# Optimization experiments

Measured on AMD Instinct MI355X. Metric: run time of the kernel, lower is better.

Reference implementation:

```python
import jax, jax.numpy as jnp
import numpy as np

N, DIM, DK, DV = 8192, 1024, 128, 128


def setup_inputs() -> dict:
    key = jax.random.key(0)
    ks = jax.random.split(key, 5)
    # Match equinox Linear init scale roughly (uniform(-1/sqrt(in), 1/sqrt(in)))
    lim = 1.0 / np.sqrt(DIM)
    return {
        "x": jax.random.normal(ks[0], (N, DIM), dtype=jnp.float32),
        "Wqk": jax.random.uniform(ks[1], (DK, DIM), jnp.float32, -lim, lim),
        "bqk": jax.random.uniform(ks[2], (DK,), jnp.float32, -lim, lim),
        "Wv": jax.random.uniform(ks[3], (DV, DIM), jnp.float32, -lim, lim),
        "bv": jax.random.uniform(ks[4], (DV,), jnp.float32, -lim, lim),
    }


def reference(x, Wqk, bqk, Wv, bv):
    # shared QK projection: q == k == x @ Wqk^T + bqk  -> [n, dk]
    qk = jnp.einsum("nd,kd->nk", x, Wqk) + bqk
    v = jnp.einsum("nd,vd->nv", x, Wv) + bv  # [n, dv]
    # full n x n score matrix (no 1/sqrt(dk) scaling in the original)
    score = jnp.einsum("ik,jk->ij", qk, qk)  # [n, n]
    score = jax.nn.softmax(score, axis=-1)
    return jnp.einsum("ij,jv->iv", score, v)  # [n, dv]
```

## Files before the change

### kernel.cpp

```cpp
#include <hip/hip_runtime.h>
#include <math.h>

#define NROWS 8192
#define DIMX  1024
#define DKV   128
#define KSPLIT 4
#define KEYS_PER_SPLIT (NROWS / KSPLIT)
#define BN 64
#define QK_SCALE 1.2011224087864498f
#define M_FIX 96.0f

typedef __attribute__((ext_vector_type(8))) short bf16x8;
typedef __attribute__((ext_vector_type(4))) short s16x4;
typedef __attribute__((ext_vector_type(4))) float f32x4;
typedef __attribute__((ext_vector_type(4))) unsigned u32x4;

static __device__ __forceinline__ short f2bf(float f) {
    union { float f; unsigned u; } v; v.f = f;
    unsigned r = v.u + 0x7fff + ((v.u >> 16) & 1);
    return (short)(r >> 16);
}

__global__ __launch_bounds__(256) void wcvt_kernel(
    const float* __restrict__ Wqk, const float* __restrict__ bqk,
    const float* __restrict__ Wv,  const float* __restrict__ bv,
    short* __restrict__ wb, float* __restrict__ bb)
{
    const int idx = blockIdx.x * 1024 + threadIdx.x * 4;
    const bool isqk = idx < DKV * DIMX;
    const float* src = isqk ? (Wqk + idx) : (Wv + (idx - DKV * DIMX));
    const float sc = isqk ? QK_SCALE : 1.0f;
    const float4 f = *(const float4*)src;
    s16x4 o;
    o.x = f2bf(f.x * sc); o.y = f2bf(f.y * sc);
    o.z = f2bf(f.z * sc); o.w = f2bf(f.w * sc);
    *(s16x4*)&wb[idx] = o;
    if (blockIdx.x == 0) {
        const int t = threadIdx.x;
        bb[t] = (t < DKV) ? bqk[t] * QK_SCALE : bv[t - DKV];
    }
}

__global__ __launch_bounds__(256) void proj_kernel(
    const float* __restrict__ x, const short* __restrict__ wb,
    const float* __restrict__ bb, short* __restrict__ qkb, short* __restrict__ vtb)
{
    __shared__ __align__(16) short xb[32 * 1024];

    const int tid  = threadIdx.x;
    const int lane = tid & 63;
    const int wave = tid >> 6;
    const int l15  = lane & 15;
    const int quad = lane >> 4;
    const int mat  = blockIdx.y;
    const int rbase = blockIdx.x * 32;
    const int wr = wave >> 1, wc = wave & 1;
    const short* wsrc = wb + (size_t)mat * DKV * DIMX;

    #pragma unroll 8
    for (int i = 0; i < 32; ++i) {
        const float4 f = *(const float4*)(x + (size_t)(rbase + i) * DIMX + tid * 4);
        s16x4 o;
        o.x = f2bf(f.x); o.y = f2bf(f.y); o.z = f2bf(f.z); o.w = f2bf(f.w);
        *(s16x4*)&xb[i * 1024 + ((tid * 4) ^ ((i & 7) << 3))] = o;
    }
    __syncthreads();

    f32x4 acc[4];
    for (int i = 0; i < 4; ++i) acc[i] = (f32x4)0.0f;

    const int arow = wr * 16 + l15;
    const int aswz = (arow & 7) << 3;
    const short* arowp = &xb[arow * 1024];

    const short* wcol[4];
    for (int nt = 0; nt < 4; ++nt)
        wcol[nt] = wsrc + (size_t)(wc * 64 + nt * 16 + l15) * DIMX + quad * 8;

    bf16x8 bA[4], bB[4];
    for (int nt = 0; nt < 4; ++nt) bA[nt] = *(const bf16x8*)(wcol[nt]);

    for (int kk = 0; kk < 32; kk += 2) {
        for (int nt = 0; nt < 4; ++nt)
            bB[nt] = *(const bf16x8*)(wcol[nt] + (kk + 1) * 32);
        const bf16x8 a0 = *(const bf16x8*)&arowp[(kk * 32 + quad * 8) ^ aswz];
        for (int nt = 0; nt < 4; ++nt)
            acc[nt] = __builtin_amdgcn_mfma_f32_16x16x32_bf16(a0, bA[nt], acc[nt], 0, 0, 0);
        if (kk + 2 < 32)
            for (int nt = 0; nt < 4; ++nt)
                bA[nt] = *(const bf16x8*)(wcol[nt] + (kk + 2) * 32);
        const bf16x8 a1 = *(const bf16x8*)&arowp[((kk + 1) * 32 + quad * 8) ^ aswz];
        for (int nt = 0; nt < 4; ++nt)
            acc[nt] = __builtin_amdgcn_mfma_f32_16x16x32_bf16(a1, bB[nt], acc[nt], 0, 0, 0);
    }

    const int rw = rbase + wr * 16 + quad * 4;
    for (int nt = 0; nt < 4; ++nt) {
        const int col = wc * 64 + nt * 16 + l15;
        const float bias = bb[mat * DKV + col];
        if (mat == 0) {
            for (int r = 0; r < 4; ++r)
                qkb[(size_t)(rw + r) * DKV + col] = f2bf(acc[nt][r] + bias);
        } else {
            s16x4 o;
            o.x = f2bf(acc[nt][0] + bias); o.y = f2bf(acc[nt][1] + bias);
            o.z = f2bf(acc[nt][2] + bias); o.w = f2bf(acc[nt][3] + bias);
            *(s16x4*)&vtb[(size_t)col * NROWS + rw] = o;
        }
    }
}

__global__ __launch_bounds__(256, 2) void flash_kernel(
    const short* __restrict__ qkb, const short* __restrict__ vtb,
    float* __restrict__ opart, float* __restrict__ lpart)
{
    __shared__ __align__(16) short kt[2][64 * 128];
    __shared__ __align__(16) short vt[2][128 * 64];

    const int tid  = threadIdx.x;
    const int lane = tid & 63;
    const int wave = tid >> 6;
    const int l15  = lane & 15;
    const int quad = lane >> 4;
    const int rg   = wave >> 1;
    const int kh   = wave & 1;
    const int rbase = blockIdx.x * 64 + rg * 32;
    const int ks = blockIdx.y;
    const int swzr = (l15 & 7) << 3;

    unsigned koff[4], voff[4];
    for (int i = 0; i < 4; ++i) {
        const int krow = wave * 16 + i * 4 + quad;
        const int s = krow & 7;
        const int srow = (krow & ~7) | (((s & 1) << 2) | (s >> 1));
        koff[i] = (unsigned)srow * 256u
                + (((unsigned)l15 * 16u) ^ (((unsigned)krow & 7u) << 4));
        const int vrow = wave * 32 + i * 8 + (lane >> 3);
        voff[i] = (unsigned)vrow * (unsigned)(NROWS * 2)
                + ((((unsigned)lane & 7u) * 16u) ^ (((unsigned)vrow & 7u) << 4));
    }

#define FL_ISSUE(buf, j0) do { \
        const char* kb_ = (const char*)qkb + (size_t)(j0) * (DKV * 2); \
        const char* vb_ = (const char*)vtb + (size_t)(j0) * 2; \
        for (int i = 0; i < 4; ++i) \
            __builtin_amdgcn_global_load_lds( \
                (const __attribute__((address_space(1))) void*)(kb_ + koff[i]), \
                (__attribute__((address_space(3))) void*)((char*)&kt[buf][0] + (wave * 4 + i) * 1024), \
                16, 0, 0); \
        for (int i = 0; i < 4; ++i) \
            __builtin_amdgcn_global_load_lds( \
                (const __attribute__((address_space(1))) void*)(vb_ + voff[i]), \
                (__attribute__((address_space(3))) void*)((char*)&vt[buf][0] + (wave * 4 + i) * 1024), \
                16, 0, 0); \
    } while (0)

    bf16x8 qf[2][4];
    #pragma unroll 2
    for (int h = 0; h < 2; ++h) {
        const short* qrow = qkb + (size_t)(rbase + h * 16 + l15) * DKV;
        for (int k = 0; k < 4; ++k)
            qf[h][k] = *(const bf16x8*)(qrow + k * 32 + quad * 8);
    }

    bf16x8 ones;
    for (int j = 0; j < 8; ++j) ones[j] = (short)0x3F80;

    f32x4 oacc[2][8];
    #pragma unroll 2
    for (int h = 0; h < 2; ++h)
        for (int i = 0; i < 8; ++i) oacc[h][i] = (f32x4)0.0f;
    f32x4 lsum[2] = {(f32x4)0.0f, (f32x4)0.0f};

    const int krow0 = kh * 32 + 2 * l15;
    const int swk0  = ((krow0 & 7) << 3);

#define TILE(CUR, NXT, j0, more) do { \
        if (more) FL_ISSUE(NXT, (j0) + BN); \
        f32x4 s[2][2]; \
        __builtin_amdgcn_s_setprio(1); \
        for (int ntl = 0; ntl < 2; ++ntl) { \
            f32x4 a0 = (f32x4)0.0f, a1 = (f32x4)0.0f; \
            const int rowb = (krow0 + ntl) * 128; \
            const int swk  = swk0 + ntl * 8; \
            for (int k_ = 0; k_ < 4; ++k_) { \
                const bf16x8 kb = *(const bf16x8*) \
                    &kt[CUR][rowb + ((k_ * 32 + quad * 8) ^ swk)]; \
                a0 = __builtin_amdgcn_mfma_f32_16x16x32_bf16(kb, qf[0][k_], a0, 0, 0, 0); \
                a1 = __builtin_amdgcn_mfma_f32_16x16x32_bf16(kb, qf[1][k_], a1, 0, 0, 0); \
            } \
            s[0][ntl] = a0; s[1][ntl] = a1; \
        } \
        __builtin_amdgcn_s_setprio(0); \
        for (int h = 0; h < 2; ++h) \
            for (int ntl = 0; ntl < 2; ++ntl) \
                for (int r = 0; r < 4; ++r) \
                    s[h][ntl][r] = __builtin_amdgcn_exp2f(s[h][ntl][r] - M_FIX); \
        bf16x8 pa[2]; \
        for (int h = 0; h < 2; ++h) { \
            u32x4 t; \
            asm("v_cvt_pk_bf16_f32 %0, %1, %2" : "=v"(t.x) : "v"(s[h][0][0]), "v"(s[h][0][1])); \
            asm("v_cvt_pk_bf16_f32 %0, %1, %2" : "=v"(t.y) : "v"(s[h][0][2]), "v"(s[h][0][3])); \
            asm("v_cvt_pk_bf16_f32 %0, %1, %2" : "=v"(t.z) : "v"(s[h][1][0]), "v"(s[h][1][1])); \
            asm("v_cvt_pk_bf16_f32 %0, %1, %2" : "=v"(t.w) : "v"(s[h][1][2]), "v"(s[h][1][3])); \
            pa[h] = *(bf16x8*)&t; \
        } \
        __builtin_amdgcn_s_setprio(1); \
        lsum[0] = __builtin_amdgcn_mfma_f32_16x16x32_bf16(pa[0], ones, lsum[0], 0, 0, 0); \
        lsum[1] = __builtin_amdgcn_mfma_f32_16x16x32_bf16(pa[1], ones, lsum[1], 0, 0, 0); \
        for (int nt_ = 0; nt_ < 8; ++nt_) { \
            const bf16x8 vb = *(const bf16x8*) \
                &vt[CUR][(nt_ * 16 + l15) * 64 + ((kh * 32 + quad * 8) ^ swzr)]; \
            oacc[0][nt_] = __builtin_amdgcn_mfma_f32_16x16x32_bf16(pa[0], vb, oacc[0][nt_], 0, 0, 0); \
            oacc[1][nt_] = __builtin_amdgcn_mfma_f32_16x16x32_bf16(pa[1], vb, oacc[1][nt_], 0, 0, 0); \
        } \
        __builtin_amdgcn_s_setprio(0); \
        __syncthreads();    \
    } while (0)

    const int j_begin = ks * KEYS_PER_SPLIT;
    const int j_end   = j_begin + KEYS_PER_SPLIT;

    FL_ISSUE(0, j_begin);
    __syncthreads();

    for (int j0 = j_begin; j0 < j_end; j0 += 2 * BN) {
        TILE(0, 1, j0, true);
        TILE(1, 0, j0 + BN, (j0 + 2 * BN) < j_end);
    }

    float* obuf = (float*)&kt[0][0] + rg * 32 * 128;
    float* lbuf = (float*)&vt[0][0];
    if (kh == 1) {
        #pragma unroll 2
        for (int h = 0; h < 2; ++h) {
            for (int nt = 0; nt < 8; ++nt)
                for (int r = 0; r < 4; ++r)
                    obuf[(h * 16 + quad * 4 + r) * 128 + nt * 16 + l15] = oacc[h][nt][r];
            if (l15 == 0)
                for (int r = 0; r < 4; ++r)
                    lbuf[rg * 32 + h * 16 + quad * 4 + r] = lsum[h][r];
        }
    }
    __syncthreads();
    if (kh == 0) {
        #pragma unroll 2
        for (int h = 0; h < 2; ++h) {
            const int rw = rbase + h * 16 + quad * 4;
            for (int nt = 0; nt < 8; ++nt) {
                const int col = nt * 16 + l15;
                for (int r = 0; r < 4; ++r)
                    opart[((size_t)ks * NROWS + rw + r) * DKV + col] =
                        oacc[h][nt][r] + obuf[(h * 16 + quad * 4 + r) * 128 + col];
            }
            if (l15 == 0)
                for (int r = 0; r < 4; ++r)
                    lpart[ks * NROWS + rw + r] =
                        lsum[h][r] + lbuf[rg * 32 + h * 16 + quad * 4 + r];
        }
    }
#undef FL_ISSUE
#undef TILE
}

__global__ __launch_bounds__(256) void combine_kernel(
    const float* __restrict__ opart, const float* __restrict__ lpart,
    float* __restrict__ out)
{
    const int idx = blockIdx.x * 256 + threadIdx.x;
    const int row = idx >> 7;
    float L = 0.f, acc = 0.f;
    for (int s = 0; s < KSPLIT; ++s) {
        L   += lpart[s * NROWS + row];
        acc += opart[(size_t)s * NROWS * DKV + idx];
    }
    out[idx] = acc / L;
}

extern "C" void kernel_launch(void* const* d_in, const int* in_sizes, int n_in,
                              void* d_out, int out_size, void* d_ws, size_t ws_size,
                              hipStream_t stream) {
    const float* x   = (const float*)d_in[0];
    const float* Wqk = (const float*)d_in[1];
    const float* bqk = (const float*)d_in[2];
    const float* Wv  = (const float*)d_in[3];
    const float* bv  = (const float*)d_in[4];
    float* out = (float*)d_out;

    char* ws = (char*)d_ws;
    short* qkb   = (short*)ws;
    short* vtb   = (short*)(ws + (2u << 20));
    short* wb    = (short*)(ws + (4u << 20));
    float* bb    = (float*)(ws + (4u << 20) + (512u << 10));
    float* opart = (float*)(ws + (5u << 20));
    float* lpart = (float*)(ws + (21u << 20));

    wcvt_kernel<<<dim3(256), 256, 0, stream>>>(Wqk, bqk, Wv, bv, wb, bb);
    proj_kernel<<<dim3(256, 2), 256, 0, stream>>>(x, wb, bb, qkb, vtb);
    flash_kernel<<<dim3(NROWS / 64, KSPLIT), 256, 0, stream>>>(qkb, vtb, opart, lpart);
    combine_kernel<<<dim3(NROWS * DKV / 256), 256, 0, stream>>>(opart, lpart, out);
}
```

Measured before the change: 156.2 us.

## Pre-swizzle V into MFMA fragment layout and load directly to registers

The projection kernel now writes V in a fragment-ordered layout matching the MFMA B-operand, so the attention kernel loads V tiles straight from global memory into registers, double-buffered across tiles. This removes the V LDS staging buffer, its global-to-LDS copies and its LDS reads, which frees shared memory and LDS bandwidth. In exchange it raises register pressure (two sets of 8 bf16x8 fragments per thread) and makes global latency visible to the PV MFMAs if the prefetch does not cover it.

```diff
diff --git a/kernel.cpp b/kernel.cpp
--- a/kernel.cpp
+++ b/kernel.cpp
@@ -43,7 +43,7 @@
 
 __global__ __launch_bounds__(256) void proj_kernel(
     const float* __restrict__ x, const short* __restrict__ wb,
-    const float* __restrict__ bb, short* __restrict__ qkb, short* __restrict__ vtb)
+    const float* __restrict__ bb, short* __restrict__ qkb, short* __restrict__ vtb2)
 {
     __shared__ __align__(16) short xb[32 * 1024];
 
@@ -95,27 +95,37 @@
     }
 
     const int rw = rbase + wr * 16 + quad * 4;
-    for (int nt = 0; nt < 4; ++nt) {
-        const int col = wc * 64 + nt * 16 + l15;
-        const float bias = bb[mat * DKV + col];
-        if (mat == 0) {
+    if (mat == 0) {
+        for (int nt = 0; nt < 4; ++nt) {
+            const int col = wc * 64 + nt * 16 + l15;
+            const float bias = bb[col];
             for (int r = 0; r < 4; ++r)
                 qkb[(size_t)(rw + r) * DKV + col] = f2bf(acc[nt][r] + bias);
-        } else {
+        }
+    } else {
+        const int Jb  = blockIdx.x >> 1;
+        const int khb = blockIdx.x & 1;
+        const int vquad = ((wr * 16 + quad * 4) >> 3) & 3;
+        const int e0 = (quad & 1) * 4;
+        for (int nt = 0; nt < 4; ++nt) {
+            const int col = wc * 64 + nt * 16 + l15;
+            const float bias = bb[DKV + col];
             s16x4 o;
             o.x = f2bf(acc[nt][0] + bias); o.y = f2bf(acc[nt][1] + bias);
             o.z = f2bf(acc[nt][2] + bias); o.w = f2bf(acc[nt][3] + bias);
-            *(s16x4*)&vtb[(size_t)col * NROWS + rw] = o;
+            short* dst = vtb2 + ((size_t)(Jb * 8 + (col >> 4)) * 2 + khb) * 512
+                       + (col & 15) * 32 + vquad * 8 + e0;
+            *(s16x4*)dst = o;
         }
     }
 }
 
 __global__ __launch_bounds__(256, 2) void flash_kernel(
-    const short* __restrict__ qkb, const short* __restrict__ vtb,
+    const short* __restrict__ qkb, const short* __restrict__ vtb2,
     float* __restrict__ opart, float* __restrict__ lpart)
 {
     __shared__ __align__(16) short kt[2][64 * 128];
-    __shared__ __align__(16) short vt[2][128 * 64];
+    __shared__ float lbuf[64];
 
     const int tid  = threadIdx.x;
     const int lane = tid & 63;
@@ -126,33 +136,30 @@
     const int kh   = wave & 1;
     const int rbase = blockIdx.x * 64 + rg * 32;
     const int ks = blockIdx.y;
-    const int swzr = (l15 & 7) << 3;
-
-    unsigned koff[4], voff[4];
+
+    unsigned koff[4];
     for (int i = 0; i < 4; ++i) {
         const int krow = wave * 16 + i * 4 + quad;
         const int s = krow & 7;
         const int srow = (krow & ~7) | (((s & 1) << 2) | (s >> 1));
         koff[i] = (unsigned)srow * 256u
                 + (((unsigned)l15 * 16u) ^ (((unsigned)krow & 7u) << 4));
-        const int vrow = wave * 32 + i * 8 + (lane >> 3);
-        voff[i] = (unsigned)vrow * (unsigned)(NROWS * 2)
-                + ((((unsigned)lane & 7u) * 16u) ^ (((unsigned)vrow & 7u) << 4));
     }
 
 #define FL_ISSUE(buf, j0) do { \
         const char* kb_ = (const char*)qkb + (size_t)(j0) * (DKV * 2); \
-        const char* vb_ = (const char*)vtb + (size_t)(j0) * 2; \
         for (int i = 0; i < 4; ++i) \
             __builtin_amdgcn_global_load_lds( \
                 (const __attribute__((address_space(1))) void*)(kb_ + koff[i]), \
                 (__attribute__((address_space(3))) void*)((char*)&kt[buf][0] + (wave * 4 + i) * 1024), \
                 16, 0, 0); \
-        for (int i = 0; i < 4; ++i) \
-            __builtin_amdgcn_global_load_lds( \
-                (const __attribute__((address_space(1))) void*)(vb_ + voff[i]), \
-                (__attribute__((address_space(3))) void*)((char*)&vt[buf][0] + (wave * 4 + i) * 1024), \
-                16, 0, 0); \
+    } while (0)
+
+    const short* vfb = vtb2 + (size_t)kh * 512 + l15 * 32 + quad * 8;
+#define LOADV(dst, j0) do { \
+        const short* vb_ = vfb + (size_t)((j0) >> 6) * (16 * 512); \
+        for (int nt_ = 0; nt_ < 8; ++nt_) \
+            dst[nt_] = *(const bf16x8*)(vb_ + nt_ * 1024); \
     } while (0)
 
     bf16x8 qf[2][4];
@@ -175,8 +182,8 @@
     const int krow0 = kh * 32 + 2 * l15;
     const int swk0  = ((krow0 & 7) << 3);
 
-#define TILE(CUR, NXT, j0, more) do { \
-        if (more) FL_ISSUE(NXT, (j0) + BN); \
+#define TILE(CUR, NXT, VC, VN, j0, more) do { \
+        if (more) { FL_ISSUE(NXT, (j0) + BN); LOADV(VN, (j0) + BN); } \
         f32x4 s[2][2]; \
         __builtin_amdgcn_s_setprio(1); \
         for (int ntl = 0; ntl < 2; ++ntl) { \
@@ -209,10 +216,8 @@
         lsum[0] = __builtin_amdgcn_mfma_f32_16x16x32_bf16(pa[0], ones, lsum[0], 0, 0, 0); \
         lsum[1] = __builtin_amdgcn_mfma_f32_16x16x32_bf16(pa[1], ones, lsum[1], 0, 0, 0); \
         for (int nt_ = 0; nt_ < 8; ++nt_) { \
-            const bf16x8 vb = *(const bf16x8*) \
-                &vt[CUR][(nt_ * 16 + l15) * 64 + ((kh * 32 + quad * 8) ^ swzr)]; \
-            oacc[0][nt_] = __builtin_amdgcn_mfma_f32_16x16x32_bf16(pa[0], vb, oacc[0][nt_], 0, 0, 0); \
-            oacc[1][nt_] = __builtin_amdgcn_mfma_f32_16x16x32_bf16(pa[1], vb, oacc[1][nt_], 0, 0, 0); \
+            oacc[0][nt_] = __builtin_amdgcn_mfma_f32_16x16x32_bf16(pa[0], VC[nt_], oacc[0][nt_], 0, 0, 0); \
+            oacc[1][nt_] = __builtin_amdgcn_mfma_f32_16x16x32_bf16(pa[1], VC[nt_], oacc[1][nt_], 0, 0, 0); \
         } \
         __builtin_amdgcn_s_setprio(0); \
         __syncthreads();    \
@@ -221,16 +226,17 @@
     const int j_begin = ks * KEYS_PER_SPLIT;
     const int j_end   = j_begin + KEYS_PER_SPLIT;
 
+    bf16x8 vfA[8], vfB[8];
     FL_ISSUE(0, j_begin);
+    LOADV(vfA, j_begin);
     __syncthreads();
 
     for (int j0 = j_begin; j0 < j_end; j0 += 2 * BN) {
-        TILE(0, 1, j0, true);
-        TILE(1, 0, j0 + BN, (j0 + 2 * BN) < j_end);
+        TILE(0, 1, vfA, vfB, j0, true);
+        TILE(1, 0, vfB, vfA, j0 + BN, (j0 + 2 * BN) < j_end);
     }
 
     float* obuf = (float*)&kt[0][0] + rg * 32 * 128;
-    float* lbuf = (float*)&vt[0][0];
     if (kh == 1) {
         #pragma unroll 2
         for (int h = 0; h < 2; ++h) {
@@ -260,6 +266,7 @@
         }
     }
 #undef FL_ISSUE
+#undef LOADV
 #undef TILE
 }
 
@@ -289,14 +296,14 @@
 
     char* ws = (char*)d_ws;
     short* qkb   = (short*)ws;
-    short* vtb   = (short*)(ws + (2u << 20));
+    short* vtb2  = (short*)(ws + (2u << 20));
     short* wb    = (short*)(ws + (4u << 20));
     float* bb    = (float*)(ws + (4u << 20) + (512u << 10));
     float* opart = (float*)(ws + (5u << 20));
     float* lpart = (float*)(ws + (21u << 20));
 
     wcvt_kernel<<<dim3(256), 256, 0, stream>>>(Wqk, bqk, Wv, bv, wb, bb);
-    proj_kernel<<<dim3(256, 2), 256, 0, stream>>>(x, wb, bb, qkb, vtb);
-    flash_kernel<<<dim3(NROWS / 64, KSPLIT), 256, 0, stream>>>(qkb, vtb, opart, lpart);
+    proj_kernel<<<dim3(256, 2), 256, 0, stream>>>(x, wb, bb, qkb, vtb2);
+    flash_kernel<<<dim3(NROWS / 64, KSPLIT), 256, 0, stream>>>(qkb, vtb2, opart, lpart);
     combine_kernel<<<dim3(NROWS * DKV / 256), 256, 0, stream>>>(opart, lpart, out);
 }
```

Measured after the change: 163.6 us. 4.7% more time.

## Restructure flash kernel to one 16-row tile per wave with BN=32 and adaptive key split

Applied to the files above, without the earlier changes.

Each wave now owns its own 16 query rows and walks all keys itself. This replaces the previous layout of two waves sharing 32 rows and splitting keys, which needed a shared-memory reduction at the end. The key tile shrinks to 32 and LDS buffers halve, which allows 4 blocks per CU, and the key split becomes 8 when the workspace is large enough. This aims to raise occupancy and parallelism and to drop the in-block reduction, at the cost of less reuse of each K/V tile across query rows, more partial-output traffic and a heavier combine pass.

```diff
diff --git a/kernel.cpp b/kernel.cpp
--- a/kernel.cpp
+++ b/kernel.cpp
@@ -4,9 +4,7 @@
 #define NROWS 8192
 #define DIMX  1024
 #define DKV   128
-#define KSPLIT 4
-#define KEYS_PER_SPLIT (NROWS / KSPLIT)
-#define BN 64
+#define BN    32
 #define QK_SCALE 1.2011224087864498f
 #define M_FIX 96.0f
 
@@ -110,116 +108,105 @@
     }
 }
 
-__global__ __launch_bounds__(256, 2) void flash_kernel(
+__global__ __launch_bounds__(256, 4) void flash_kernel(
     const short* __restrict__ qkb, const short* __restrict__ vtb,
-    float* __restrict__ opart, float* __restrict__ lpart)
-{
-    __shared__ __align__(16) short kt[2][64 * 128];
-    __shared__ __align__(16) short vt[2][128 * 64];
+    float* __restrict__ opart, float* __restrict__ lpart, int kps)
+{
+    __shared__ __align__(16) short kt[2][32 * 128];
+    __shared__ __align__(16) short vt[2][128 * 32];
 
     const int tid  = threadIdx.x;
     const int lane = tid & 63;
     const int wave = tid >> 6;
     const int l15  = lane & 15;
     const int quad = lane >> 4;
-    const int rg   = wave >> 1;
-    const int kh   = wave & 1;
-    const int rbase = blockIdx.x * 64 + rg * 32;
-    const int ks = blockIdx.y;
-    const int swzr = (l15 & 7) << 3;
-
-    unsigned koff[4], voff[4];
-    for (int i = 0; i < 4; ++i) {
-        const int krow = wave * 16 + i * 4 + quad;
-        const int s = krow & 7;
-        const int srow = (krow & ~7) | (((s & 1) << 2) | (s >> 1));
-        koff[i] = (unsigned)srow * 256u
+    const int rbase = blockIdx.x * 64 + wave * 16;
+    const int ksid = blockIdx.y;
+
+    unsigned koff[2], voff[2];
+    for (int i = 0; i < 2; ++i) {
+        const int krow = wave * 8 + i * 4 + quad;
+        const int g = krow >> 4, p = krow & 15;
+        const int srck = 8 * (p >> 2) + 4 * g + (p & 3);
+        koff[i] = (unsigned)srck * 256u
                 + (((unsigned)l15 * 16u) ^ (((unsigned)krow & 7u) << 4));
-        const int vrow = wave * 32 + i * 8 + (lane >> 3);
-        voff[i] = (unsigned)vrow * (unsigned)(NROWS * 2)
-                + ((((unsigned)lane & 7u) * 16u) ^ (((unsigned)vrow & 7u) << 4));
+        const int d = wave * 32 + i * 16 + (lane >> 2);
+        voff[i] = (unsigned)d * (unsigned)(NROWS * 2)
+                + ((((unsigned)lane & 3u) * 16u) ^ (((unsigned)d & 3u) << 4));
     }
 
 #define FL_ISSUE(buf, j0) do { \
         const char* kb_ = (const char*)qkb + (size_t)(j0) * (DKV * 2); \
         const char* vb_ = (const char*)vtb + (size_t)(j0) * 2; \
-        for (int i = 0; i < 4; ++i) \
+        for (int i = 0; i < 2; ++i) \
             __builtin_amdgcn_global_load_lds( \
                 (const __attribute__((address_space(1))) void*)(kb_ + koff[i]), \
-                (__attribute__((address_space(3))) void*)((char*)&kt[buf][0] + (wave * 4 + i) * 1024), \
+                (__attribute__((address_space(3))) void*)((char*)&kt[buf][0] + (wave * 2 + i) * 1024), \
                 16, 0, 0); \
-        for (int i = 0; i < 4; ++i) \
+        for (int i = 0; i < 2; ++i) \
             __builtin_amdgcn_global_load_lds( \
                 (const __attribute__((address_space(1))) void*)(vb_ + voff[i]), \
-                (__attribute__((address_space(3))) void*)((char*)&vt[buf][0] + (wave * 4 + i) * 1024), \
+                (__attribute__((address_space(3))) void*)((char*)&vt[buf][0] + (wave * 2 + i) * 1024), \
                 16, 0, 0); \
     } while (0)
 
-    bf16x8 qf[2][4];
-    #pragma unroll 2
-    for (int h = 0; h < 2; ++h) {
-        const short* qrow = qkb + (size_t)(rbase + h * 16 + l15) * DKV;
+    bf16x8 qf[4];
+    {
+        const short* qrow = qkb + (size_t)(rbase + l15) * DKV;
         for (int k = 0; k < 4; ++k)
-            qf[h][k] = *(const bf16x8*)(qrow + k * 32 + quad * 8);
+            qf[k] = *(const bf16x8*)(qrow + k * 32 + quad * 8);
     }
 
     bf16x8 ones;
     for (int j = 0; j < 8; ++j) ones[j] = (short)0x3F80;
 
-    f32x4 oacc[2][8];
-    #pragma unroll 2
-    for (int h = 0; h < 2; ++h)
-        for (int i = 0; i < 8; ++i) oacc[h][i] = (f32x4)0.0f;
-    f32x4 lsum[2] = {(f32x4)0.0f, (f32x4)0.0f};
-
-    const int krow0 = kh * 32 + 2 * l15;
-    const int swk0  = ((krow0 & 7) << 3);
+    f32x4 oacc[8];
+    for (int i = 0; i < 8; ++i) oacc[i] = (f32x4)0.0f;
+    f32x4 lsum = (f32x4)0.0f;
+
+    const int swzk = (l15 & 7) << 3;
+    const int swzv = (l15 & 3) << 3;
 
 #define TILE(CUR, NXT, j0, more) do { \
         if (more) FL_ISSUE(NXT, (j0) + BN); \
-        f32x4 s[2][2]; \
+        f32x4 s[2]; \
         __builtin_amdgcn_s_setprio(1); \
-        for (int ntl = 0; ntl < 2; ++ntl) { \
-            f32x4 a0 = (f32x4)0.0f, a1 = (f32x4)0.0f; \
-            const int rowb = (krow0 + ntl) * 128; \
-            const int swk  = swk0 + ntl * 8; \
+        for (int g = 0; g < 2; ++g) { \
+            f32x4 a = (f32x4)0.0f; \
+            const int rowb = (g * 16 + l15) * 128; \
             for (int k_ = 0; k_ < 4; ++k_) { \
                 const bf16x8 kb = *(const bf16x8*) \
-                    &kt[CUR][rowb + ((k_ * 32 + quad * 8) ^ swk)]; \
-                a0 = __builtin_amdgcn_mfma_f32_16x16x32_bf16(kb, qf[0][k_], a0, 0, 0, 0); \
-                a1 = __builtin_amdgcn_mfma_f32_16x16x32_bf16(kb, qf[1][k_], a1, 0, 0, 0); \
+                    &kt[CUR][rowb + ((k_ * 32 + quad * 8) ^ swzk)]; \
+                a = __builtin_amdgcn_mfma_f32_16x16x32_bf16(kb, qf[k_], a, 0, 0, 0); \
             } \
-            s[0][ntl] = a0; s[1][ntl] = a1; \
+            s[g] = a; \
         } \
         __builtin_amdgcn_s_setprio(0); \
-        for (int h = 0; h < 2; ++h) \
-            for (int ntl = 0; ntl < 2; ++ntl) \
-                for (int r = 0; r < 4; ++r) \
-                    s[h][ntl][r] = __builtin_amdgcn_exp2f(s[h][ntl][r] - M_FIX); \
-        bf16x8 pa[2]; \
-        for (int h = 0; h < 2; ++h) { \
+        for (int g = 0; g < 2; ++g) \
+            for (int r = 0; r < 4; ++r) \
+                s[g][r] = __builtin_amdgcn_exp2f(s[g][r] - M_FIX); \
+        bf16x8 pa; \
+        { \
             u32x4 t; \
-            asm("v_cvt_pk_bf16_f32 %0, %1, %2" : "=v"(t.x) : "v"(s[h][0][0]), "v"(s[h][0][1])); \
-            asm("v_cvt_pk_bf16_f32 %0, %1, %2" : "=v"(t.y) : "v"(s[h][0][2]), "v"(s[h][0][3])); \
-            asm("v_cvt_pk_bf16_f32 %0, %1, %2" : "=v"(t.z) : "v"(s[h][1][0]), "v"(s[h][1][1])); \
-            asm("v_cvt_pk_bf16_f32 %0, %1, %2" : "=v"(t.w) : "v"(s[h][1][2]), "v"(s[h][1][3])); \
-            pa[h] = *(bf16x8*)&t; \
+            asm("v_cvt_pk_bf16_f32 %0, %1, %2" : "=v"(t.x) : "v"(s[0][0]), "v"(s[0][1])); \
+            asm("v_cvt_pk_bf16_f32 %0, %1, %2" : "=v"(t.y) : "v"(s[0][2]), "v"(s[0][3])); \
+            asm("v_cvt_pk_bf16_f32 %0, %1, %2" : "=v"(t.z) : "v"(s[1][0]), "v"(s[1][1])); \
+            asm("v_cvt_pk_bf16_f32 %0, %1, %2" : "=v"(t.w) : "v"(s[1][2]), "v"(s[1][3])); \
+            pa = *(bf16x8*)&t; \
         } \
         __builtin_amdgcn_s_setprio(1); \
-        lsum[0] = __builtin_amdgcn_mfma_f32_16x16x32_bf16(pa[0], ones, lsum[0], 0, 0, 0); \
-        lsum[1] = __builtin_amdgcn_mfma_f32_16x16x32_bf16(pa[1], ones, lsum[1], 0, 0, 0); \
+        lsum = __builtin_amdgcn_mfma_f32_16x16x32_bf16(pa, ones, lsum, 0, 0, 0); \
         for (int nt_ = 0; nt_ < 8; ++nt_) { \
             const bf16x8 vb = *(const bf16x8*) \
-                &vt[CUR][(nt_ * 16 + l15) * 64 + ((kh * 32 + quad * 8) ^ swzr)]; \
-            oacc[0][nt_] = __builtin_amdgcn_mfma_f32_16x16x32_bf16(pa[0], vb, oacc[0][nt_], 0, 0, 0); \
-            oacc[1][nt_] = __builtin_amdgcn_mfma_f32_16x16x32_bf16(pa[1], vb, oacc[1][nt_], 0, 0, 0); \
+                &vt[CUR][(nt_ * 16 + l15) * 32 + ((quad * 8) ^ swzv)]; \
+            oacc[nt_] = __builtin_amdgcn_mfma_f32_16x16x32_bf16(pa, vb, oacc[nt_], 0, 0, 0); \
         } \
         __builtin_amdgcn_s_setprio(0); \
         __syncthreads();    \
     } while (0)
 
-    const int j_begin = ks * KEYS_PER_SPLIT;
-    const int j_end   = j_begin + KEYS_PER_SPLIT;
+    const int j_begin = ksid * kps;
+    const int j_end   = j_begin + kps;
 
     FL_ISSUE(0, j_begin);
     __syncthreads();
@@ -229,48 +216,27 @@
         TILE(1, 0, j0 + BN, (j0 + 2 * BN) < j_end);
     }
 
-    float* obuf = (float*)&kt[0][0] + rg * 32 * 128;
-    float* lbuf = (float*)&vt[0][0];
-    if (kh == 1) {
-        #pragma unroll 2
-        for (int h = 0; h < 2; ++h) {
-            for (int nt = 0; nt < 8; ++nt)
-                for (int r = 0; r < 4; ++r)
-                    obuf[(h * 16 + quad * 4 + r) * 128 + nt * 16 + l15] = oacc[h][nt][r];
-            if (l15 == 0)
-                for (int r = 0; r < 4; ++r)
-                    lbuf[rg * 32 + h * 16 + quad * 4 + r] = lsum[h][r];
-        }
-    }
-    __syncthreads();
-    if (kh == 0) {
-        #pragma unroll 2
-        for (int h = 0; h < 2; ++h) {
-            const int rw = rbase + h * 16 + quad * 4;
-            for (int nt = 0; nt < 8; ++nt) {
-                const int col = nt * 16 + l15;
-                for (int r = 0; r < 4; ++r)
-                    opart[((size_t)ks * NROWS + rw + r) * DKV + col] =
-                        oacc[h][nt][r] + obuf[(h * 16 + quad * 4 + r) * 128 + col];
-            }
-            if (l15 == 0)
-                for (int r = 0; r < 4; ++r)
-                    lpart[ks * NROWS + rw + r] =
-                        lsum[h][r] + lbuf[rg * 32 + h * 16 + quad * 4 + r];
-        }
-    }
+    const int rw = rbase + quad * 4;
+    for (int nt = 0; nt < 8; ++nt) {
+        const int col = nt * 16 + l15;
+        for (int r = 0; r < 4; ++r)
+            opart[((size_t)ksid * NROWS + rw + r) * DKV + col] = oacc[nt][r];
+    }
+    if (l15 == 0)
+        for (int r = 0; r < 4; ++r)
+            lpart[ksid * NROWS + rw + r] = lsum[r];
 #undef FL_ISSUE
 #undef TILE
 }
 
 __global__ __launch_bounds__(256) void combine_kernel(
     const float* __restrict__ opart, const float* __restrict__ lpart,
-    float* __restrict__ out)
+    float* __restrict__ out, int ks)
 {
     const int idx = blockIdx.x * 256 + threadIdx.x;
     const int row = idx >> 7;
     float L = 0.f, acc = 0.f;
-    for (int s = 0; s < KSPLIT; ++s) {
+    for (int s = 0; s < ks; ++s) {
         L   += lpart[s * NROWS + row];
         acc += opart[(size_t)s * NROWS * DKV + idx];
     }
@@ -293,10 +259,13 @@
     short* wb    = (short*)(ws + (4u << 20));
     float* bb    = (float*)(ws + (4u << 20) + (512u << 10));
     float* opart = (float*)(ws + (5u << 20));
-    float* lpart = (float*)(ws + (21u << 20));
+
+    const size_t need8 = (5ull << 20) + (32ull << 20) + (256ull << 10);
+    const int ks = (ws_size >= need8) ? 8 : 4;
+    float* lpart = (float*)(ws + (5u << 20) + (size_t)ks * (4u << 20));
 
     wcvt_kernel<<<dim3(256), 256, 0, stream>>>(Wqk, bqk, Wv, bv, wb, bb);
     proj_kernel<<<dim3(256, 2), 256, 0, stream>>>(x, wb, bb, qkb, vtb);
-    flash_kernel<<<dim3(NROWS / 64, KSPLIT), 256, 0, stream>>>(qkb, vtb, opart, lpart);
-    combine_kernel<<<dim3(NROWS * DKV / 256), 256, 0, stream>>>(opart, lpart, out);
-}
+    flash_kernel<<<dim3(NROWS / 64, ks), 256, 0, stream>>>(qkb, vtb, opart, lpart, NROWS / ks);
+    combine_kernel<<<dim3(NROWS * DKV / 256), 256, 0, stream>>>(opart, lpart, out, ks);
+}
```

Result: slower. 163.6 us (+4.7%).

## Halve key tile to 32, raise flash occupancy, use 8-way key split when workspace allows

Applied to the files above, without the earlier changes.

Shrinks the key tile from 64 to 32 so the double-buffered LDS footprint drops to about 33KB, and raises launch bounds to 4 blocks per CU. The P·V and row-sum MFMAs switch to the 16x16x16 bf16 variant with new LDS swizzles for the narrower K and V tiles. The key dimension split goes from 4 to 8 when the workspace is large enough, which adds more blocks for latency hiding. In exchange there are more barriers per key, smaller MFMA instructions, register pressure under the tighter launch bound, and more partial output traffic in the combine step.

```diff
diff --git a/kernel.cpp b/kernel.cpp
--- a/kernel.cpp
+++ b/kernel.cpp
@@ -4,16 +4,14 @@
 #define NROWS 8192
 #define DIMX  1024
 #define DKV   128
-#define KSPLIT 4
-#define KEYS_PER_SPLIT (NROWS / KSPLIT)
-#define BN 64
+#define BN    32
 #define QK_SCALE 1.2011224087864498f
 #define M_FIX 96.0f
 
 typedef __attribute__((ext_vector_type(8))) short bf16x8;
 typedef __attribute__((ext_vector_type(4))) short s16x4;
 typedef __attribute__((ext_vector_type(4))) float f32x4;
-typedef __attribute__((ext_vector_type(4))) unsigned u32x4;
+typedef __attribute__((ext_vector_type(2))) unsigned u32x2;
 
 static __device__ __forceinline__ short f2bf(float f) {
     union { float f; unsigned u; } v; v.f = f;
@@ -110,12 +108,14 @@
     }
 }
 
-__global__ __launch_bounds__(256, 2) void flash_kernel(
+__global__ __launch_bounds__(256, 4) void flash_kernel(
     const short* __restrict__ qkb, const short* __restrict__ vtb,
-    float* __restrict__ opart, float* __restrict__ lpart)
+    float* __restrict__ opart, float* __restrict__ lpart, int kps)
 {
-    __shared__ __align__(16) short kt[2][64 * 128];
-    __shared__ __align__(16) short vt[2][128 * 64];
+    __shared__ __align__(16) char smem[33280];
+    short* ktp = (short*)smem;
+    short* vtp = (short*)(smem + 16384);
+    float* lbuf = (float*)(smem + 32768);
 
     const int tid  = threadIdx.x;
     const int lane = tid & 63;
@@ -125,33 +125,30 @@
     const int rg   = wave >> 1;
     const int kh   = wave & 1;
     const int rbase = blockIdx.x * 64 + rg * 32;
-    const int ks = blockIdx.y;
-    const int swzr = (l15 & 7) << 3;
-
-    unsigned koff[4], voff[4];
-    for (int i = 0; i < 4; ++i) {
-        const int krow = wave * 16 + i * 4 + quad;
-        const int s = krow & 7;
-        const int srow = (krow & ~7) | (((s & 1) << 2) | (s >> 1));
-        koff[i] = (unsigned)srow * 256u
+    const int ksid = blockIdx.y;
+
+    unsigned koff[2], voff[2];
+    for (int i = 0; i < 2; ++i) {
+        const int krow = wave * 8 + i * 4 + quad;
+        koff[i] = (unsigned)krow * 256u
                 + (((unsigned)l15 * 16u) ^ (((unsigned)krow & 7u) << 4));
-        const int vrow = wave * 32 + i * 8 + (lane >> 3);
-        voff[i] = (unsigned)vrow * (unsigned)(NROWS * 2)
-                + ((((unsigned)lane & 7u) * 16u) ^ (((unsigned)vrow & 7u) << 4));
+        const int dv = wave * 32 + i * 16 + (lane >> 2);
+        voff[i] = (unsigned)dv * (unsigned)(NROWS * 2)
+                + ((((unsigned)lane & 3u) ^ ((unsigned)dv & 3u)) * 16u);
     }
 
 #define FL_ISSUE(buf, j0) do { \
         const char* kb_ = (const char*)qkb + (size_t)(j0) * (DKV * 2); \
         const char* vb_ = (const char*)vtb + (size_t)(j0) * 2; \
-        for (int i = 0; i < 4; ++i) \
+        for (int i = 0; i < 2; ++i) \
             __builtin_amdgcn_global_load_lds( \
                 (const __attribute__((address_space(1))) void*)(kb_ + koff[i]), \
-                (__attribute__((address_space(3))) void*)((char*)&kt[buf][0] + (wave * 4 + i) * 1024), \
+                (__attribute__((address_space(3))) void*)((char*)(ktp + (size_t)(buf) * 4096) + (wave * 2 + i) * 1024), \
                 16, 0, 0); \
-        for (int i = 0; i < 4; ++i) \
+        for (int i = 0; i < 2; ++i) \
             __builtin_amdgcn_global_load_lds( \
                 (const __attribute__((address_space(1))) void*)(vb_ + voff[i]), \
-                (__attribute__((address_space(3))) void*)((char*)&vt[buf][0] + (wave * 4 + i) * 1024), \
+                (__attribute__((address_space(3))) void*)((char*)(vtp + (size_t)(buf) * 4096) + (wave * 2 + i) * 1024), \
                 16, 0, 0); \
     } while (0)
 
@@ -163,8 +160,9 @@
             qf[h][k] = *(const bf16x8*)(qrow + k * 32 + quad * 8);
     }
 
-    bf16x8 ones;
-    for (int j = 0; j < 8; ++j) ones[j] = (short)0x3F80;
+    s16x4 ones4;
+    ones4.x = (short)0x3F80; ones4.y = (short)0x3F80;
+    ones4.z = (short)0x3F80; ones4.w = (short)0x3F80;
 
     f32x4 oacc[2][8];
     #pragma unroll 2
@@ -172,54 +170,53 @@
         for (int i = 0; i < 8; ++i) oacc[h][i] = (f32x4)0.0f;
     f32x4 lsum[2] = {(f32x4)0.0f, (f32x4)0.0f};
 
-    const int krow0 = kh * 32 + 2 * l15;
-    const int swk0  = ((krow0 & 7) << 3);
+    const int krd  = (kh * 16 + l15) * 128;
+    const int kxor = (l15 & 7) << 3;
+    const int vunit0 = 2 * kh + (quad >> 1);
+    const int vsub   = (quad & 1) * 8;
 
 #define TILE(CUR, NXT, j0, more) do { \
         if (more) FL_ISSUE(NXT, (j0) + BN); \
-        f32x4 s[2][2]; \
+        const short* ktc = ktp + (CUR) * 4096; \
+        const short* vtc = vtp + (CUR) * 4096; \
+        f32x4 s[2]; \
         __builtin_amdgcn_s_setprio(1); \
-        for (int ntl = 0; ntl < 2; ++ntl) { \
+        { \
             f32x4 a0 = (f32x4)0.0f, a1 = (f32x4)0.0f; \
-            const int rowb = (krow0 + ntl) * 128; \
-            const int swk  = swk0 + ntl * 8; \
             for (int k_ = 0; k_ < 4; ++k_) { \
-                const bf16x8 kb = *(const bf16x8*) \
-                    &kt[CUR][rowb + ((k_ * 32 + quad * 8) ^ swk)]; \
+                const bf16x8 kb = *(const bf16x8*)&ktc[krd + (((k_ * 4 + quad) << 3) ^ kxor)]; \
                 a0 = __builtin_amdgcn_mfma_f32_16x16x32_bf16(kb, qf[0][k_], a0, 0, 0, 0); \
                 a1 = __builtin_amdgcn_mfma_f32_16x16x32_bf16(kb, qf[1][k_], a1, 0, 0, 0); \
             } \
-            s[0][ntl] = a0; s[1][ntl] = a1; \
+            s[0] = a0; s[1] = a1; \
         } \
         __builtin_amdgcn_s_setprio(0); \
         for (int h = 0; h < 2; ++h) \
-            for (int ntl = 0; ntl < 2; ++ntl) \
-                for (int r = 0; r < 4; ++r) \
-                    s[h][ntl][r] = __builtin_amdgcn_exp2f(s[h][ntl][r] - M_FIX); \
-        bf16x8 pa[2]; \
+            for (int r = 0; r < 4; ++r) \
+                s[h][r] = __builtin_amdgcn_exp2f(s[h][r] - M_FIX); \
+        s16x4 pa[2]; \
         for (int h = 0; h < 2; ++h) { \
-            u32x4 t; \
-            asm("v_cvt_pk_bf16_f32 %0, %1, %2" : "=v"(t.x) : "v"(s[h][0][0]), "v"(s[h][0][1])); \
-            asm("v_cvt_pk_bf16_f32 %0, %1, %2" : "=v"(t.y) : "v"(s[h][0][2]), "v"(s[h][0][3])); \
-            asm("v_cvt_pk_bf16_f32 %0, %1, %2" : "=v"(t.z) : "v"(s[h][1][0]), "v"(s[h][1][1])); \
-            asm("v_cvt_pk_bf16_f32 %0, %1, %2" : "=v"(t.w) : "v"(s[h][1][2]), "v"(s[h][1][3])); \
-            pa[h] = *(bf16x8*)&t; \
+            u32x2 t; \
+            asm("v_cvt_pk_bf16_f32 %0, %1, %2" : "=v"(t.x) : "v"(s[h][0]), "v"(s[h][1])); \
+            asm("v_cvt_pk_bf16_f32 %0, %1, %2" : "=v"(t.y) : "v"(s[h][2]), "v"(s[h][3])); \
+            pa[h] = *(s16x4*)&t; \
         } \
         __builtin_amdgcn_s_setprio(1); \
-        lsum[0] = __builtin_amdgcn_mfma_f32_16x16x32_bf16(pa[0], ones, lsum[0], 0, 0, 0); \
-        lsum[1] = __builtin_amdgcn_mfma_f32_16x16x32_bf16(pa[1], ones, lsum[1], 0, 0, 0); \
+        lsum[0] = __builtin_amdgcn_mfma_f32_16x16x16bf16_1k(pa[0], ones4, lsum[0], 0, 0, 0); \
+        lsum[1] = __builtin_amdgcn_mfma_f32_16x16x16bf16_1k(pa[1], ones4, lsum[1], 0, 0, 0); \
         for (int nt_ = 0; nt_ < 8; ++nt_) { \
-            const bf16x8 vb = *(const bf16x8*) \
-                &vt[CUR][(nt_ * 16 + l15) * 64 + ((kh * 32 + quad * 8) ^ swzr)]; \
-            oacc[0][nt_] = __builtin_amdgcn_mfma_f32_16x16x32_bf16(pa[0], vb, oacc[0][nt_], 0, 0, 0); \
-            oacc[1][nt_] = __builtin_amdgcn_mfma_f32_16x16x32_bf16(pa[1], vb, oacc[1][nt_], 0, 0, 0); \
+            const int d_ = nt_ * 16 + l15; \
+            const s16x4 vb = *(const s16x4*)((const char*)vtc + d_ * 64 \
+                                + ((vunit0 ^ (l15 & 3)) << 4) + vsub); \
+            oacc[0][nt_] = __builtin_amdgcn_mfma_f32_16x16x16bf16_1k(pa[0], vb, oacc[0][nt_], 0, 0, 0); \
+            oacc[1][nt_] = __builtin_amdgcn_mfma_f32_16x16x16bf16_1k(pa[1], vb, oacc[1][nt_], 0, 0, 0); \
         } \
         __builtin_amdgcn_s_setprio(0); \
         __syncthreads();    \
     } while (0)
 
-    const int j_begin = ks * KEYS_PER_SPLIT;
-    const int j_end   = j_begin + KEYS_PER_SPLIT;
+    const int j_begin = ksid * kps;
+    const int j_end   = j_begin + kps;
 
     FL_ISSUE(0, j_begin);
     __syncthreads();
@@ -229,8 +226,7 @@
         TILE(1, 0, j0 + BN, (j0 + 2 * BN) < j_end);
     }
 
-    float* obuf = (float*)&kt[0][0] + rg * 32 * 128;
-    float* lbuf = (float*)&vt[0][0];
+    float* obuf = (float*)smem + rg * 32 * 128;
     if (kh == 1) {
         #pragma unroll 2
         for (int h = 0; h < 2; ++h) {
@@ -250,12 +246,12 @@
             for (int nt = 0; nt < 8; ++nt) {
                 const int col = nt * 16 + l15;
                 for (int r = 0; r < 4; ++r)
-                    opart[((size_t)ks * NROWS + rw + r) * DKV + col] =
+                    opart[((size_t)ksid * NROWS + rw + r) * DKV + col] =
                         oacc[h][nt][r] + obuf[(h * 16 + quad * 4 + r) * 128 + col];
             }
             if (l15 == 0)
                 for (int r = 0; r < 4; ++r)
-                    lpart[ks * NROWS + rw + r] =
+                    lpart[ksid * NROWS + rw + r] =
                         lsum[h][r] + lbuf[rg * 32 + h * 16 + quad * 4 + r];
         }
     }
@@ -265,12 +261,12 @@
 
 __global__ __launch_bounds__(256) void combine_kernel(
     const float* __restrict__ opart, const float* __restrict__ lpart,
-    float* __restrict__ out)
+    float* __restrict__ out, int ks)
 {
     const int idx = blockIdx.x * 256 + threadIdx.x;
     const int row = idx >> 7;
     float L = 0.f, acc = 0.f;
-    for (int s = 0; s < KSPLIT; ++s) {
+    for (int s = 0; s < ks; ++s) {
         L   += lpart[s * NROWS + row];
         acc += opart[(size_t)s * NROWS * DKV + idx];
     }
@@ -293,10 +289,13 @@
     short* wb    = (short*)(ws + (4u << 20));
     float* bb    = (float*)(ws + (4u << 20) + (512u << 10));
     float* opart = (float*)(ws + (5u << 20));
-    float* lpart = (float*)(ws + (21u << 20));
+
+    const size_t need8 = (5ull << 20) + (32ull << 20) + (256ull << 10);
+    const int ks = (ws_size >= need8) ? 8 : 4;
+    float* lpart = (float*)(ws + (5u << 20) + (size_t)ks * (4u << 20));
 
     wcvt_kernel<<<dim3(256), 256, 0, stream>>>(Wqk, bqk, Wv, bv, wb, bb);
     proj_kernel<<<dim3(256, 2), 256, 0, stream>>>(x, wb, bb, qkb, vtb);
-    flash_kernel<<<dim3(NROWS / 64, KSPLIT), 256, 0, stream>>>(qkb, vtb, opart, lpart);
-    combine_kernel<<<dim3(NROWS * DKV / 256), 256, 0, stream>>>(opart, lpart, out);
-}
+    flash_kernel<<<dim3(NROWS / 64, ks), 256, 0, stream>>>(qkb, vtb, opart, lpart, NROWS / ks);
+    combine_kernel<<<dim3(NROWS * DKV / 256), 256, 0, stream>>>(opart, lpart, out, ks);
+}
```

New measurement: 197.1 us. 26.2% more time.
